# Kernel tuning notes

Measured on AMD Instinct MI355X. Metric: run time of the kernel, lower is better.

The kernel has to match this reference:

```python
import jax, jax.numpy as jnp
import numpy as np

FACTOR = 1.0
KERNEL = 3
PAD = 1
STRIDE = 1


def setup_inputs() -> dict:
    key = jax.random.key(0)
    ks = jax.random.split(key, 7)
    B_, Cin, Cout, L, CODE = 32, 128, 128, 4096, 2
    return {
        "input": jax.random.normal(ks[0], (B_, Cin, L), dtype=jnp.float32),
        "codes": jax.random.normal(ks[1], (B_, CODE, CODE), dtype=jnp.float32),
        "weight": jax.random.normal(ks[2], (Cout, Cin, KERNEL), dtype=jnp.float32) * 0.05,
        "A": jax.random.normal(ks[3], (Cin, CODE, KERNEL), dtype=jnp.float32) * 0.05,
        "B": jax.random.normal(ks[4], (Cout, CODE, KERNEL), dtype=jnp.float32) * 0.05,
        "bias": jax.random.normal(ks[5], (Cout,), dtype=jnp.float32) * 0.05,
        "bias_context": jax.random.normal(ks[6], (CODE, Cout), dtype=jnp.float32) * 0.05,
    }


def reference(input, codes, weight, A, B, bias, bias_context):
    # Hypernetwork-generated per-sample conv weights (low-rank via codes)
    w = jnp.einsum('ick,bcr->birk', A, codes)            # (b, in, code, k)
    context_w = jnp.einsum('birk,ork->boik', w, B)       # (b, out, in, k)
    combined_weight = weight + FACTOR * context_w        # (b, out, in, k)

    diag = jnp.diagonal(codes, axis1=-2, axis2=-1)       # (b, code)
    context_bias = diag @ bias_context                   # (b, out)
    combined_bias = bias + FACTOR * context_bias         # (b, out)

    # circular padding along spatial axis
    padded = jnp.pad(input, ((0, 0), (0, 0), (PAD, PAD)), mode='wrap')
    L_out = (input.shape[-1] + 2 * PAD - KERNEL) // STRIDE + 1
    # windowed view: (b, in, L_out, k) via k shifted slices (k is tiny, loop ok)
    windows = jnp.stack([padded[:, :, j:j + L_out * STRIDE:STRIDE] for j in range(KERNEL)], axis=-1)
    out = jnp.einsum('bihw,boiw->boh', windows, combined_weight)
    return out + combined_bias[..., None]
```

## Files before the change

### kernel.cpp

```cpp
#include <hip/hip_runtime.h>
#include <hip/hip_bf16.h>
#include <stdint.h>
#include <stddef.h>

#define L_LEN 4096
#define CIN   128
#define COUT  128
#define NB    32
#define KTOT  384
#define TN    64
#define ROWS  (TN + 2)

typedef __bf16 bf16x8 __attribute__((ext_vector_type(8)));
typedef float  f32x4  __attribute__((ext_vector_type(4)));

__device__ __forceinline__ uint16_t f2bf(float f) {
    union { float f; uint32_t u; } v; v.f = f;
    return (uint16_t)((v.u + 0x7fffu + ((v.u >> 16) & 1u)) >> 16);
}
__device__ __forceinline__ uint32_t pack2(float lo, float hi) {
    return (uint32_t)f2bf(lo) | ((uint32_t)f2bf(hi) << 16);
}

__global__ __launch_bounds__(256) void geps_combine(
    const float* __restrict__ codes, const float* __restrict__ weight,
    const float* __restrict__ Amat,  const float* __restrict__ Bmat,
    const float* __restrict__ bias,  const float* __restrict__ bias_ctx,
    uint16_t* __restrict__ Wc, float* __restrict__ cbias)
{
    int tid = blockIdx.x * 256 + threadIdx.x;
    if (tid < NB * COUT * KTOT) {
        int j    = tid & 7;
        int lane = (tid >> 3) & 63;
        int mt   = (tid >> 9) & 1;
        int tmp  = tid >> 10;
        int t    = tmp % 12;
        int bo   = tmp / 12;
        int og   = bo & 3;
        int b    = bo >> 2;
        int col  = t * 32 + (lane >> 4) * 8 + j;
        int k    = col >> 7;
        int i    = col & 127;
        int o    = og * 32 + mt * 16 + (lane & 15);
        float cw = 0.f;
        #pragma unroll
        for (int c = 0; c < 2; ++c) {
            float a = Amat[i * 6 + c * 3 + k];
            #pragma unroll
            for (int r = 0; r < 2; ++r)
                cw += a * codes[b * 4 + c * 2 + r] * Bmat[o * 6 + r * 3 + k];
        }
        float val = weight[o * 384 + i * 3 + k] + cw;
        Wc[tid] = f2bf(val);
    }
    if (tid < NB * COUT) {
        int b = tid >> 7, o = tid & 127;
        float cb = bias[o];
        #pragma unroll
        for (int c = 0; c < 2; ++c)
            cb += codes[b * 4 + c * 2 + c] * bias_ctx[c * 128 + o];
        cbias[tid] = cb;
    }
}

__global__ __launch_bounds__(256, 4) void geps_conv(
    const float* __restrict__ in, const uint16_t* __restrict__ Wc,
    const float* __restrict__ cbias, float* __restrict__ out)
{
    __shared__ uint16_t __attribute__((aligned(16))) Xt[ROWS * 128];
    __shared__ float cb[COUT];

    const int tid  = threadIdx.x;
    const int b    = blockIdx.y;
    const int h0   = blockIdx.x * TN;
    const int lane = tid & 63;
    const int wid  = tid >> 6;
    const int m16  = lane & 15;
    const int q    = lane >> 4;
    const int mq   = wid * 32;

    if (tid < COUT) cb[tid] = cbias[b * COUT + tid];

    const float* inb = in + (size_t)b * CIN * L_LEN;

    const uint16_t* WcW = Wc + (size_t)(b * 4 + wid) * 12288 + lane * 8;
    bf16x8 ac0 = *(const bf16x8*)(WcW);
    bf16x8 ac1 = *(const bf16x8*)(WcW + 512);

    #pragma unroll
    for (int it = 0; it < 2; ++it) {
        int task = it * 256 + tid;
        int p4   = task >> 4;
        int qd   = task & 15;
        const float* r0 = inb + (size_t)(4 * p4) * L_LEN + h0 + 4 * qd;
        float4 a0 = *(const float4*)(r0);
        float4 a1 = *(const float4*)(r0 + L_LEN);
        float4 a2 = *(const float4*)(r0 + 2 * L_LEN);
        float4 a3 = *(const float4*)(r0 + 3 * L_LEN);
        const int off = (4 * p4) & 7;
        const int pc  = p4 >> 1;
        const float v0[4] = {a0.x, a0.y, a0.z, a0.w};
        const float v1[4] = {a1.x, a1.y, a1.z, a1.w};
        const float v2[4] = {a2.x, a2.y, a2.z, a2.w};
        const float v3[4] = {a3.x, a3.y, a3.z, a3.w};
        #pragma unroll
        for (int j = 0; j < 4; ++j) {
            int r  = 1 + 4 * qd + j;
            int ch = pc ^ (r & 15);
            uint2 w;
            w.x = pack2(v0[j], v1[j]);
            w.y = pack2(v2[j], v3[j]);
            *(uint2*)&Xt[r * 128 + (ch << 3) + off] = w;
        }
    }
    if (tid < 128) {
        int p    = tid & 63;
        int side = tid >> 6;
        int r    = side ? (ROWS - 1) : 0;
        int gh   = (h0 - 1 + r) & (L_LEN - 1);
        float x0 = inb[(size_t)(2 * p)     * L_LEN + gh];
        float x1 = inb[(size_t)(2 * p + 1) * L_LEN + gh];
        int chunk = (p >> 2) ^ (r & 15);
        *(uint32_t*)&Xt[r * 128 + (chunk << 3) + ((2 * p) & 7)] = pack2(x0, x1);
    }

    f32x4 acc[2][4];
    #pragma unroll
    for (int a = 0; a < 2; ++a)
        #pragma unroll
        for (int c = 0; c < 4; ++c) acc[a][c] = 0.0f;

    __syncthreads();

    #pragma unroll 1
    for (int t = 0; t < 12; ++t) {
        const uint16_t* pn = WcW + ((t + 1 < 12) ? (t + 1) : 11) * 1024;
        bf16x8 an0 = *(const bf16x8*)(pn);
        bf16x8 an1 = *(const bf16x8*)(pn + 512);

        const int k   = t >> 2;
        const int i0c = (t & 3) << 2;
        bf16x8 bf[4];
        #pragma unroll
        for (int nt = 0; nt < 4; ++nt) {
            int r  = nt * 16 + m16 + k;
            int ch = (i0c + q) ^ (r & 15);
            bf[nt] = *(const bf16x8*)&Xt[r * 128 + (ch << 3)];
        }
        #pragma unroll
        for (int nt = 0; nt < 4; ++nt) {
            acc[0][nt] = __builtin_amdgcn_mfma_f32_16x16x32_bf16(ac0, bf[nt], acc[0][nt], 0, 0, 0);
            acc[1][nt] = __builtin_amdgcn_mfma_f32_16x16x32_bf16(ac1, bf[nt], acc[1][nt], 0, 0, 0);
        }
        ac0 = an0; ac1 = an1;
    }

    float* outb = out + (size_t)b * COUT * L_LEN + h0;
    #pragma unroll
    for (int mt = 0; mt < 2; ++mt) {
        #pragma unroll
        for (int reg = 0; reg < 4; ++reg) {
            int o = mq + mt * 16 + q * 4 + reg;
            float bv = cb[o];
            float* orow = outb + (size_t)o * L_LEN;
            #pragma unroll
            for (int nt = 0; nt < 4; ++nt)
                __builtin_nontemporal_store(acc[mt][nt][reg] + bv,
                                            &orow[nt * 16 + m16]);
        }
    }
}

extern "C" void kernel_launch(void* const* d_in, const int* in_sizes, int n_in,
                              void* d_out, int out_size, void* d_ws, size_t ws_size,
                              hipStream_t stream) {
    const float* input    = (const float*)d_in[0];
    const float* codes    = (const float*)d_in[1];
    const float* weight   = (const float*)d_in[2];
    const float* Amat     = (const float*)d_in[3];
    const float* Bmat     = (const float*)d_in[4];
    const float* bias     = (const float*)d_in[5];
    const float* bias_ctx = (const float*)d_in[6];
    float* out = (float*)d_out;

    uint16_t* Wc    = (uint16_t*)d_ws;
    float*    cbias = (float*)((char*)d_ws + (size_t)NB * COUT * KTOT * 2);

    geps_combine<<<dim3((NB * COUT * KTOT) / 256), 256, 0, stream>>>(
        codes, weight, Amat, Bmat, bias, bias_ctx, Wc, cbias);
    geps_conv<<<dim3(L_LEN / TN, NB), 256, 0, stream>>>(input, Wc, cbias, out);
}
```

Measured before the change: 138.5 us.

## Process four spatial tiles per block with register-resident weights and double-buffered LDS

Each conv block now handles four consecutive 64-wide spatial tiles. The full per-wave weight fragment (12x2 bf16x8) is loaded into registers once and reused across the tiles. The next tile's input is prefetched into registers while the current tile's MFMAs run, then packed into a second LDS buffer. This amortizes weight loads and block setup and overlaps global loads with compute. In exchange it uses more registers (occupancy hint lowered to 2), a larger LDS footprint, and a quarter as many blocks (512 total).

After: 140.9 us. About the same (+1.7%).

```diff
diff --git a/kernel.cpp b/kernel.cpp
--- a/kernel.cpp
+++ b/kernel.cpp
@@ -9,6 +9,7 @@
 #define NB    32
 #define KTOT  384
 #define TN    64
+#define TPB   4
 #define ROWS  (TN + 2)
 
 typedef __bf16 bf16x8 __attribute__((ext_vector_type(8)));
@@ -63,16 +64,72 @@
     }
 }
 
-__global__ __launch_bounds__(256, 4) void geps_conv(
+#define LOAD_TILE(H0)                                                        \
+    {                                                                        \
+        const float* tb = inb + (H0);                                        \
+        _Pragma("unroll")                                                    \
+        for (int it = 0; it < 2; ++it) {                                     \
+            int task = it * 256 + tid;                                       \
+            int p4   = task >> 4;                                            \
+            int qd   = task & 15;                                            \
+            const float* r0 = tb + (size_t)(4 * p4) * L_LEN + 4 * qd;        \
+            st[it][0] = *(const float4*)(r0);                                \
+            st[it][1] = *(const float4*)(r0 + L_LEN);                        \
+            st[it][2] = *(const float4*)(r0 + 2 * L_LEN);                    \
+            st[it][3] = *(const float4*)(r0 + 3 * L_LEN);                    \
+        }                                                                    \
+        if (tid < 128) {                                                     \
+            int p    = tid & 63;                                             \
+            int side = tid >> 6;                                             \
+            int r    = side ? (ROWS - 1) : 0;                                \
+            int gh   = ((H0) - 1 + r) & (L_LEN - 1);                         \
+            hx0 = inb[(size_t)(2 * p) * L_LEN + gh];                         \
+            hx1 = inb[(size_t)(2 * p + 1) * L_LEN + gh];                     \
+        }                                                                    \
+    }
+
+#define PACK_TILE(XP)                                                        \
+    {                                                                        \
+        uint16_t* Xw = (XP);                                                 \
+        _Pragma("unroll")                                                    \
+        for (int it = 0; it < 2; ++it) {                                     \
+            int task = it * 256 + tid;                                       \
+            int p4   = task >> 4;                                            \
+            int qd   = task & 15;                                            \
+            const int off = (4 * p4) & 7;                                    \
+            const int pc  = p4 >> 1;                                         \
+            _Pragma("unroll")                                                \
+            for (int j4 = 0; j4 < 4; ++j4) {                                 \
+                int r  = 1 + 4 * qd + j4;                                    \
+                int ch = pc ^ (r & 15);                                      \
+                uint2 w;                                                     \
+                w.x = pack2(((const float*)&st[it][0])[j4],                  \
+                            ((const float*)&st[it][1])[j4]);                 \
+                w.y = pack2(((const float*)&st[it][2])[j4],                  \
+                            ((const float*)&st[it][3])[j4]);                 \
+                *(uint2*)&Xw[r * 128 + (ch << 3) + off] = w;                 \
+            }                                                                \
+        }                                                                    \
+        if (tid < 128) {                                                     \
+            int p     = tid & 63;                                            \
+            int side  = tid >> 6;                                            \
+            int r     = side ? (ROWS - 1) : 0;                               \
+            int chunk = (p >> 2) ^ (r & 15);                                 \
+            *(uint32_t*)&Xw[r * 128 + (chunk << 3) + ((2 * p) & 7)] =        \
+                pack2(hx0, hx1);                                             \
+        }                                                                    \
+    }
+
+__global__ __launch_bounds__(256, 2) void geps_conv(
     const float* __restrict__ in, const uint16_t* __restrict__ Wc,
     const float* __restrict__ cbias, float* __restrict__ out)
 {
-    __shared__ uint16_t __attribute__((aligned(16))) Xt[ROWS * 128];
+    __shared__ uint16_t __attribute__((aligned(16))) Xt[2][ROWS * 128];
     __shared__ float cb[COUT];
 
     const int tid  = threadIdx.x;
     const int b    = blockIdx.y;
-    const int h0   = blockIdx.x * TN;
+    const int hb   = blockIdx.x * (TN * TPB);
     const int lane = tid & 63;
     const int wid  = tid >> 6;
     const int m16  = lane & 15;
@@ -84,89 +141,73 @@
     const float* inb = in + (size_t)b * CIN * L_LEN;
 
     const uint16_t* WcW = Wc + (size_t)(b * 4 + wid) * 12288 + lane * 8;
-    bf16x8 ac0 = *(const bf16x8*)(WcW);
-    bf16x8 ac1 = *(const bf16x8*)(WcW + 512);
-
+    bf16x8 af[12][2];
     #pragma unroll
-    for (int it = 0; it < 2; ++it) {
-        int task = it * 256 + tid;
-        int p4   = task >> 4;
-        int qd   = task & 15;
-        const float* r0 = inb + (size_t)(4 * p4) * L_LEN + h0 + 4 * qd;
-        float4 a0 = *(const float4*)(r0);
-        float4 a1 = *(const float4*)(r0 + L_LEN);
-        float4 a2 = *(const float4*)(r0 + 2 * L_LEN);
-        float4 a3 = *(const float4*)(r0 + 3 * L_LEN);
-        const int off = (4 * p4) & 7;
-        const int pc  = p4 >> 1;
-        const float v0[4] = {a0.x, a0.y, a0.z, a0.w};
-        const float v1[4] = {a1.x, a1.y, a1.z, a1.w};
-        const float v2[4] = {a2.x, a2.y, a2.z, a2.w};
-        const float v3[4] = {a3.x, a3.y, a3.z, a3.w};
-        #pragma unroll
-        for (int j = 0; j < 4; ++j) {
-            int r  = 1 + 4 * qd + j;
-            int ch = pc ^ (r & 15);
-            uint2 w;
-            w.x = pack2(v0[j], v1[j]);
-            w.y = pack2(v2[j], v3[j]);
-            *(uint2*)&Xt[r * 128 + (ch << 3) + off] = w;
-        }
-    }
-    if (tid < 128) {
-        int p    = tid & 63;
-        int side = tid >> 6;
-        int r    = side ? (ROWS - 1) : 0;
-        int gh   = (h0 - 1 + r) & (L_LEN - 1);
-        float x0 = inb[(size_t)(2 * p)     * L_LEN + gh];
-        float x1 = inb[(size_t)(2 * p + 1) * L_LEN + gh];
-        int chunk = (p >> 2) ^ (r & 15);
-        *(uint32_t*)&Xt[r * 128 + (chunk << 3) + ((2 * p) & 7)] = pack2(x0, x1);
-    }
+    for (int t = 0; t < 12; ++t) {
+        af[t][0] = *(const bf16x8*)(WcW + t * 1024);
+        af[t][1] = *(const bf16x8*)(WcW + t * 1024 + 512);
+    }
+
+    float4 st[2][4];
+    float  hx0 = 0.f, hx1 = 0.f;
+
+    LOAD_TILE(hb)
+    PACK_TILE(&Xt[0][0])
+    __syncthreads();
 
     f32x4 acc[2][4];
-    #pragma unroll
-    for (int a = 0; a < 2; ++a)
-        #pragma unroll
-        for (int c = 0; c < 4; ++c) acc[a][c] = 0.0f;
-
-    __syncthreads();
 
     #pragma unroll 1
-    for (int t = 0; t < 12; ++t) {
-        const uint16_t* pn = WcW + ((t + 1 < 12) ? (t + 1) : 11) * 1024;
-        bf16x8 an0 = *(const bf16x8*)(pn);
-        bf16x8 an1 = *(const bf16x8*)(pn + 512);
-
-        const int k   = t >> 2;
-        const int i0c = (t & 3) << 2;
-        bf16x8 bf[4];
-        #pragma unroll
-        for (int nt = 0; nt < 4; ++nt) {
-            int r  = nt * 16 + m16 + k;
-            int ch = (i0c + q) ^ (r & 15);
-            bf[nt] = *(const bf16x8*)&Xt[r * 128 + (ch << 3)];
-        }
-        #pragma unroll
-        for (int nt = 0; nt < 4; ++nt) {
-            acc[0][nt] = __builtin_amdgcn_mfma_f32_16x16x32_bf16(ac0, bf[nt], acc[0][nt], 0, 0, 0);
-            acc[1][nt] = __builtin_amdgcn_mfma_f32_16x16x32_bf16(ac1, bf[nt], acc[1][nt], 0, 0, 0);
-        }
-        ac0 = an0; ac1 = an1;
-    }
-
-    float* outb = out + (size_t)b * COUT * L_LEN + h0;
-    #pragma unroll
-    for (int mt = 0; mt < 2; ++mt) {
-        #pragma unroll
-        for (int reg = 0; reg < 4; ++reg) {
-            int o = mq + mt * 16 + q * 4 + reg;
-            float bv = cb[o];
-            float* orow = outb + (size_t)o * L_LEN;
-            #pragma unroll
-            for (int nt = 0; nt < 4; ++nt)
-                __builtin_nontemporal_store(acc[mt][nt][reg] + bv,
-                                            &orow[nt * 16 + m16]);
+    for (int j = 0; j < TPB; ++j) {
+        const int h0 = hb + j * TN;
+        const uint16_t* X = &Xt[j & 1][0];
+
+        if (j + 1 < TPB) LOAD_TILE(h0 + TN)
+        asm volatile("" ::: "memory");
+
+        #pragma unroll
+        for (int a = 0; a < 2; ++a)
+            #pragma unroll
+            for (int c = 0; c < 4; ++c) acc[a][c] = 0.0f;
+
+        #pragma unroll
+        for (int t = 0; t < 12; ++t) {
+            const int k   = t >> 2;
+            const int i0c = (t & 3) << 2;
+            bf16x8 bfv[4];
+            #pragma unroll
+            for (int nt = 0; nt < 4; ++nt) {
+                int r  = nt * 16 + m16 + k;
+                int ch = (i0c + q) ^ (r & 15);
+                bfv[nt] = *(const bf16x8*)&X[r * 128 + (ch << 3)];
+            }
+            #pragma unroll
+            for (int nt = 0; nt < 4; ++nt) {
+                acc[0][nt] = __builtin_amdgcn_mfma_f32_16x16x32_bf16(
+                    af[t][0], bfv[nt], acc[0][nt], 0, 0, 0);
+                acc[1][nt] = __builtin_amdgcn_mfma_f32_16x16x32_bf16(
+                    af[t][1], bfv[nt], acc[1][nt], 0, 0, 0);
+            }
+        }
+
+        float* outb = out + (size_t)b * COUT * L_LEN + h0;
+        #pragma unroll
+        for (int mt = 0; mt < 2; ++mt) {
+            #pragma unroll
+            for (int reg = 0; reg < 4; ++reg) {
+                int o = mq + mt * 16 + q * 4 + reg;
+                float bv = cb[o];
+                float* orow = outb + (size_t)o * L_LEN;
+                #pragma unroll
+                for (int nt = 0; nt < 4; ++nt)
+                    __builtin_nontemporal_store(acc[mt][nt][reg] + bv,
+                                                &orow[nt * 16 + m16]);
+            }
+        }
+
+        if (j + 1 < TPB) {
+            PACK_TILE(&Xt[(j + 1) & 1][0])
+            __syncthreads();
         }
     }
 }
@@ -188,5 +229,6 @@
 
     geps_combine<<<dim3((NB * COUT * KTOT) / 256), 256, 0, stream>>>(
         codes, weight, Amat, Bmat, bias, bias_ctx, Wc, cbias);
-    geps_conv<<<dim3(L_LEN / TN, NB), 256, 0, stream>>>(input, Wc, cbias, out);
-}
+    geps_conv<<<dim3(L_LEN / (TN * TPB), NB), 256, 0, stream>>>(
+        input, Wc, cbias, out);
+}
```
